# Performance work log

Hardware: AMD Instinct MI355X
Metric: run time of the kernel (lower is better)

Reference implementation:

```python
import jax, jax.numpy as jnp
import numpy as np

DIM = 1024
HEADS = 16
DIM_HEAD = 64
INNER = HEADS * DIM_HEAD
EPS = 1e-6


def elu_feature_map(t):
    # F.elu(x) + 1
    return jnp.where(t > 0, t + 1.0, jnp.exp(t))


def setup_inputs() -> dict:
    key = jax.random.key(0)
    k1, k2, k3, k4 = jax.random.split(key, 4)
    B, N = 4, 8192
    x = jax.random.normal(k1, (B, N, DIM), dtype=jnp.float32)
    s_in = 1.0 / np.sqrt(DIM)
    s_out = 1.0 / np.sqrt(INNER)
    Wqkv = jax.random.uniform(k2, (DIM, 3 * INNER), dtype=jnp.float32, minval=-s_in, maxval=s_in)
    Wout = jax.random.uniform(k3, (INNER, DIM), dtype=jnp.float32, minval=-s_out, maxval=s_out)
    bout = jax.random.uniform(k4, (DIM,), dtype=jnp.float32, minval=-s_out, maxval=s_out)
    return {"x": x, "Wqkv": Wqkv, "Wout": Wout, "bout": bout}


def reference(x, Wqkv, Wout, bout):
    B, N, D = x.shape
    qkv = x @ Wqkv  # [B,N,3*INNER]
    q, k, v = jnp.split(qkv, 3, axis=-1)
    # b n (h d) -> b h n d
    resh = lambda t: t.reshape(B, N, HEADS, DIM_HEAD).transpose(0, 2, 1, 3)
    q, k, v = resh(q), resh(k), resh(v)
    q = elu_feature_map(q)
    k = elu_feature_map(k)
    kv = jnp.einsum('bhnd,bhnf->bhdf', k, v)          # [B,H,d,d]
    k_sum = k.sum(axis=-2)                             # [B,H,d]
    qkv_out = jnp.einsum('bhnd,bhdf->bhnf', q, kv)    # [B,H,N,d]
    q_k_sum = jnp.einsum('bhnd,bhd->bhn', q, k_sum)   # [B,H,N]
    out = qkv_out / (q_k_sum[..., None] + EPS)
    out = out.transpose(0, 2, 1, 3).reshape(B, N, INNER)  # b h n d -> b n (h d)
    return out @ Wout + bout
```

## Files before the change

### kernel.cpp

```cpp
#include <hip/hip_runtime.h>
#include <hip/hip_bf16.h>
#include <math.h>


typedef unsigned short ushort_t;
typedef __attribute__((ext_vector_type(8))) short s8v;
typedef __attribute__((ext_vector_type(4))) float f32x4;

#define MFMA(a,b,c) __builtin_amdgcn_mfma_f32_16x16x32_bf16((a),(b),(c),0,0,0)

typedef __attribute__((address_space(3))) unsigned int as3_u32;
typedef __attribute__((address_space(1))) const unsigned int as1_u32c;

__device__ __forceinline__ void g2l16(const void* g, void* l) {
    __builtin_amdgcn_global_load_lds((as1_u32c*)g, (as3_u32*)l, 16, 0, 0);
}

__device__ __forceinline__ float bf2f(ushort_t u) {
    union { float f; unsigned v; } x; x.v = ((unsigned)u) << 16; return x.f;
}
__device__ __forceinline__ ushort_t f2bf(float f) {
    union { float f; unsigned v; } x; x.f = f;
    unsigned r = x.v + 0x7fffu + ((x.v >> 16) & 1u);
    return (ushort_t)(r >> 16);
}
__device__ __forceinline__ float elu1(float t) { return t > 0.0f ? t + 1.0f : expf(t); }

__global__ void k_cast(const float* __restrict__ in, ushort_t* __restrict__ out, int n8) {
    int i = blockIdx.x * blockDim.x + threadIdx.x;
    if (i >= n8) return;
    const float4* p = (const float4*)in;
    float4 a = p[(size_t)i * 2], b = p[(size_t)i * 2 + 1];
    uint4 o;
    o.x = (unsigned)f2bf(a.x) | ((unsigned)f2bf(a.y) << 16);
    o.y = (unsigned)f2bf(a.z) | ((unsigned)f2bf(a.w) << 16);
    o.z = (unsigned)f2bf(b.x) | ((unsigned)f2bf(b.y) << 16);
    o.w = (unsigned)f2bf(b.z) | ((unsigned)f2bf(b.w) << 16);
    *(uint4*)(out + (size_t)i * 8) = o;
}

__global__ __launch_bounds__(256) void k_transpose(const float* __restrict__ W,
                                                   ushort_t* __restrict__ WT, int K, int N) {
    __shared__ float s[32][33];
    const int t = threadIdx.x;
    const int k0 = blockIdx.x * 32, n0 = blockIdx.y * 32;
    const int kr = t >> 3, n4 = (t & 7) * 4;
    float4 v = *(const float4*)(W + (size_t)(k0 + kr) * N + n0 + n4);
    s[kr][n4 + 0] = v.x; s[kr][n4 + 1] = v.y; s[kr][n4 + 2] = v.z; s[kr][n4 + 3] = v.w;
    __syncthreads();
    const int nr = kr, k4 = n4;
    unsigned lo = (unsigned)f2bf(s[k4 + 0][nr]) | ((unsigned)f2bf(s[k4 + 1][nr]) << 16);
    unsigned hi = (unsigned)f2bf(s[k4 + 2][nr]) | ((unsigned)f2bf(s[k4 + 3][nr]) << 16);
    *(uint2*)(WT + (size_t)(n0 + nr) * K + k0 + k4) = make_uint2(lo, hi);
}

template<int MODE>
__global__ __launch_bounds__(512, 2) void k_gemm(
    const ushort_t* __restrict__ A, const ushort_t* __restrict__ B,
    ushort_t* __restrict__ obf, const float* __restrict__ bout, float* __restrict__ of)
{
    constexpr int ASZ  = 256 * 64;
    constexpr int BUFS = 2 * ASZ;
    __shared__ ushort_t lds[2 * BUFS];

    const int t = threadIdx.x, l = t & 63, w = t >> 6;
    const int wr = w >> 2, wc = w & 3;
    const size_t m0 = (size_t)blockIdx.x * 256;
    const size_t n0 = (size_t)blockIdx.y * 256;

    f32x4 acc[8][4];
    const f32x4 z = {0.f, 0.f, 0.f, 0.f};
#pragma unroll
    for (int i = 0; i < 8; i++)
#pragma unroll
        for (int j = 0; j < 4; j++) acc[i][j] = z;

    const int lr  = l >> 3;
    const int lco = ((l & 7) ^ lr) << 3;
    const ushort_t* gA = A + (m0 + (size_t)(32 * w) + lr) * 1024 + lco;
    const ushort_t* gB = B + (n0 + (size_t)(32 * w) + lr) * 1024 + lco;
    const int la15 = l & 15;
    const int exo  = (((l >> 4) ^ (l & 7)) << 3);

#pragma unroll
    for (int i = 0; i < 4; i++)
        g2l16(gA + (size_t)(8 * i) * 1024, &lds[(w * 4 + i) * 512]);
#pragma unroll
    for (int i = 0; i < 4; i++)
        g2l16(gB + (size_t)(8 * i) * 1024, &lds[ASZ + (w * 4 + i) * 512]);
    asm volatile("s_waitcnt vmcnt(0)" ::: "memory");
    __builtin_amdgcn_sched_barrier(0);
    __builtin_amdgcn_s_barrier();
    __builtin_amdgcn_sched_barrier(0);

    for (int T = 0; T < 16; ++T) {
        const int base  = (T & 1) * BUFS;
        const int nbase = BUFS - base;

        if (T < 15) {
            const size_t k1 = (size_t)(T + 1) * 64;
#pragma unroll
            for (int i = 0; i < 4; i++)
                g2l16(gA + (size_t)(8 * i) * 1024 + k1, &lds[nbase + (w * 4 + i) * 512]);
#pragma unroll
            for (int i = 0; i < 4; i++)
                g2l16(gB + (size_t)(8 * i) * 1024 + k1, &lds[nbase + ASZ + (w * 4 + i) * 512]);
        }

        s8v af[8], bf[4];
#pragma unroll
        for (int nf = 0; nf < 4; nf++)
            bf[nf] = *(const s8v*)&lds[base + ASZ + (wc * 64 + nf * 16 + la15) * 64 + exo];
#pragma unroll
        for (int mf = 0; mf < 8; mf++)
            af[mf] = *(const s8v*)&lds[base + (wr * 128 + mf * 16 + la15) * 64 + exo];
        __builtin_amdgcn_s_setprio(1);
#pragma unroll
        for (int mf = 0; mf < 8; mf++)
#pragma unroll
            for (int nf = 0; nf < 4; nf++)
                acc[mf][nf] = MFMA(af[mf], bf[nf], acc[mf][nf]);
        __builtin_amdgcn_s_setprio(0);
#pragma unroll
        for (int nf = 0; nf < 4; nf++)
            bf[nf] = *(const s8v*)&lds[base + ASZ + (wc * 64 + nf * 16 + la15) * 64 + (32 ^ exo)];
#pragma unroll
        for (int mf = 0; mf < 8; mf++)
            af[mf] = *(const s8v*)&lds[base + (wr * 128 + mf * 16 + la15) * 64 + (32 ^ exo)];
        __builtin_amdgcn_s_setprio(1);
#pragma unroll
        for (int mf = 0; mf < 8; mf++)
#pragma unroll
            for (int nf = 0; nf < 4; nf++)
                acc[mf][nf] = MFMA(af[mf], bf[nf], acc[mf][nf]);
        __builtin_amdgcn_s_setprio(0);

        if (T < 15) {
            __builtin_amdgcn_sched_barrier(0);
            asm volatile("s_waitcnt vmcnt(0)" ::: "memory");
            __builtin_amdgcn_sched_barrier(0);
            __builtin_amdgcn_s_barrier();
            __builtin_amdgcn_sched_barrier(0);
        }
    }

    const int r4 = (l >> 4) * 4;
    if (MODE == 0) {
#pragma unroll
        for (int mf = 0; mf < 8; mf++)
#pragma unroll
            for (int nf = 0; nf < 4; nf++) {
                const size_t colb = n0 + wc * 64 + nf * 16;
                const bool feat = colb < 2048;
#pragma unroll
                for (int r = 0; r < 4; r++) {
                    const size_t row = m0 + wr * 128 + mf * 16 + r4 + r;
                    float v = acc[mf][nf][r];
                    obf[row * 3072 + colb + la15] = f2bf(feat ? elu1(v) : v);
                }
            }
    } else {
#pragma unroll
        for (int mf = 0; mf < 8; mf++)
#pragma unroll
            for (int nf = 0; nf < 4; nf++) {
                const size_t col = n0 + wc * 64 + nf * 16 + la15;
                const float bo = bout[col];
#pragma unroll
                for (int r = 0; r < 4; r++) {
                    const size_t row = m0 + wr * 128 + mf * 16 + r4 + r;
                    of[row * 1024 + col] = acc[mf][nf][r] + bo;
                }
            }
    }
}

#define KST 136
__global__ __launch_bounds__(256) void k_kv(
    const ushort_t* __restrict__ qkv, float* __restrict__ kv, float* __restrict__ ksum)
{
    __shared__ ushort_t kT[64 * KST];
    __shared__ ushort_t vT[64 * KST];
    __shared__ float ksl[64];
    const int t = threadIdx.x, l = t & 63, w = t >> 6;
    const int wr = w >> 1, wc = w & 1;
    const int h = blockIdx.x;
    const int b = blockIdx.z;
    const ushort_t* qkvb = qkv + (size_t)b * 8192 * 3072;
    float* kvh = kv + ((size_t)b * 16 + h) * 4096;
    float* ksh = ksum + (size_t)b * 1024 + h * 64;
    const int n00 = blockIdx.y * 512;
    const f32x4 z = {0.f, 0.f, 0.f, 0.f};
    f32x4 acc[2][2] = {{z, z}, {z, z}};
    float ksloc[4] = {0.f, 0.f, 0.f, 0.f};
    const int sd0 = (t & 15) * 4;
    if (t < 64) ksl[t] = 0.f;

    for (int c = 0; c < 4; c++) {
        __syncthreads();
        const int n0 = n00 + c * 128;
#pragma unroll
        for (int i = 0; i < 8; i++) {
            int n = i * 16 + (t >> 4);
            const ushort_t* kp = qkvb + (size_t)(n0 + n) * 3072 + 1024 + h * 64 + sd0;
            ushort4 kw = *(const ushort4*)kp;
            ushort4 vw = *(const ushort4*)(kp + 1024);
            ksloc[0] += bf2f(kw.x); ksloc[1] += bf2f(kw.y);
            ksloc[2] += bf2f(kw.z); ksloc[3] += bf2f(kw.w);
            kT[(sd0 + 0) * KST + n] = kw.x; kT[(sd0 + 1) * KST + n] = kw.y;
            kT[(sd0 + 2) * KST + n] = kw.z; kT[(sd0 + 3) * KST + n] = kw.w;
            vT[(sd0 + 0) * KST + n] = vw.x; vT[(sd0 + 1) * KST + n] = vw.y;
            vT[(sd0 + 2) * KST + n] = vw.z; vT[(sd0 + 3) * KST + n] = vw.w;
        }
        __syncthreads();
#pragma unroll
        for (int kb = 0; kb < 128; kb += 32) {
            s8v af[2], bfr[2];
#pragma unroll
            for (int ma = 0; ma < 2; ma++) {
                int d = wr * 32 + ma * 16 + (l & 15);
                af[ma] = *(const s8v*)&kT[d * KST + kb + (l >> 4) * 8];
            }
#pragma unroll
            for (int fb = 0; fb < 2; fb++) {
                int f = wc * 32 + fb * 16 + (l & 15);
                bfr[fb] = *(const s8v*)&vT[f * KST + kb + (l >> 4) * 8];
            }
#pragma unroll
            for (int ma = 0; ma < 2; ma++)
#pragma unroll
                for (int fb = 0; fb < 2; fb++)
                    acc[ma][fb] = MFMA(af[ma], bfr[fb], acc[ma][fb]);
        }
    }
    atomicAdd(&ksl[sd0 + 0], ksloc[0]); atomicAdd(&ksl[sd0 + 1], ksloc[1]);
    atomicAdd(&ksl[sd0 + 2], ksloc[2]); atomicAdd(&ksl[sd0 + 3], ksloc[3]);
    __syncthreads();
    if (t < 64) atomicAdd(&ksh[t], ksl[t]);
#pragma unroll
    for (int ma = 0; ma < 2; ma++)
#pragma unroll
        for (int fb = 0; fb < 2; fb++)
#pragma unroll
            for (int r = 0; r < 4; r++) {
                int d = wr * 32 + ma * 16 + (l >> 4) * 4 + r;
                int f = wc * 32 + fb * 16 + (l & 15);
                atomicAdd(&kvh[f * 64 + d], acc[ma][fb][r]);
            }
}

#define AST 72
__global__ __launch_bounds__(256) void k_apply(
    const ushort_t* __restrict__ qkv, const float* __restrict__ kv,
    const float* __restrict__ ksum, ushort_t* __restrict__ attn)
{
    __shared__ ushort_t kvb[64 * AST];
    const int t = threadIdx.x, l = t & 63, w = t >> 6;
    const int la15 = l & 15;
    const int row0 = blockIdx.x * 32;
    const int b = row0 >> 13;
    const f32x4 z = {0.f, 0.f, 0.f, 0.f};

    for (int hh = 0; hh < 8; hh++) {
        const int h = blockIdx.y * 8 + hh;
        const float* kvh = kv + ((size_t)b * 16 + h) * 4096;
        const float* ksh = ksum + (size_t)b * 1024 + h * 64;
        __syncthreads();
        {
            const int f = t >> 2, d0 = (t & 3) * 16;
            const float* src = kvh + f * 64 + d0;
            s8v v0, v1;
#pragma unroll
            for (int j = 0; j < 8; j++) {
                v0[j] = (short)f2bf(src[j]);
                v1[j] = (short)f2bf(src[j + 8]);
            }
            *(s8v*)&kvb[f * AST + d0]     = v0;
            *(s8v*)&kvb[f * AST + d0 + 8] = v1;
        }
        __syncthreads();
        float ksv[16];
        {
            const float* kp = ksh + (l >> 4) * 8;
            *(float4*)&ksv[0]  = *(const float4*)(kp);
            *(float4*)&ksv[4]  = *(const float4*)(kp + 4);
            *(float4*)&ksv[8]  = *(const float4*)(kp + 32);
            *(float4*)&ksv[12] = *(const float4*)(kp + 36);
        }
        f32x4 acc[2] = {z, z};
        float pd[2] = {0.f, 0.f};
#pragma unroll
        for (int ks = 0; ks < 2; ks++) {
            const int f = w * 16 + la15;
            s8v bfr = *(const s8v*)&kvb[f * AST + ks * 32 + (l >> 4) * 8];
#pragma unroll
            for (int ma = 0; ma < 2; ma++) {
                int row = row0 + ma * 16 + la15;
                s8v afr = *(const s8v*)(qkv + (size_t)row * 3072 + h * 64 + ks * 32 + (l >> 4) * 8);
#pragma unroll
                for (int j = 0; j < 8; j++)
                    pd[ma] += bf2f((ushort_t)afr[j]) * ksv[ks * 8 + j];
                acc[ma] = MFMA(afr, bfr, acc[ma]);
            }
        }
#pragma unroll
        for (int ma = 0; ma < 2; ma++) {
            pd[ma] += __shfl_xor(pd[ma], 16, 64);
            pd[ma] += __shfl_xor(pd[ma], 32, 64);
        }
#pragma unroll
        for (int ma = 0; ma < 2; ma++)
#pragma unroll
            for (int r = 0; r < 4; r++) {
                int lrow = (l >> 4) * 4 + r;
                float dot = __shfl(pd[ma], lrow, 64);
                float dv = 1.f / (dot + 1e-6f);
                int row = row0 + ma * 16 + lrow;
                int f = w * 16 + la15;
                attn[(size_t)row * 1024 + h * 64 + f] = f2bf(acc[ma][r] * dv);
            }
    }
}

extern "C" void kernel_launch(void* const* d_in, const int* in_sizes, int n_in,
                              void* d_out, int out_size, void* d_ws, size_t ws_size,
                              hipStream_t stream) {
    const float* x    = (const float*)d_in[0];
    const float* Wqkv = (const float*)d_in[1];
    const float* Wout = (const float*)d_in[2];
    const float* bout = (const float*)d_in[3];
    float* out = (float*)d_out;
    char* ws = (char*)d_ws;

    ushort_t* WqkvT = (ushort_t*)(ws + 0);
    ushort_t* WoutT = (ushort_t*)(ws + 6291456);
    float*    kv    = (float*)(ws + 8388608);
    float*    ksum  = (float*)(ws + 12582912);
    ushort_t* xb    = (ushort_t*)(ws + 12599296);
    ushort_t* qkv   = (ushort_t*)(ws + 79708160);
    ushort_t* attn  = (ushort_t*)(ws + 281034752);

    k_transpose<<<dim3(32, 96), 256, 0, stream>>>(Wqkv, WqkvT, 1024, 3072);
    k_transpose<<<dim3(32, 32), 256, 0, stream>>>(Wout, WoutT, 1024, 1024);
    hipMemsetAsync(kv, 0, 4194304 + 16384, stream);
    k_cast<<<16384, 256, 0, stream>>>(x, xb, 4194304);

    k_gemm<0><<<dim3(128, 12), 512, 0, stream>>>(xb, WqkvT, qkv, nullptr, nullptr);
    k_kv<<<dim3(16, 16, 4), 256, 0, stream>>>(qkv, kv, ksum);
    k_apply<<<dim3(1024, 2), 256, 0, stream>>>(qkv, kv, ksum, attn);
    k_gemm<1><<<dim3(128, 4), 512, 0, stream>>>(attn, WoutT, nullptr, bout, out);
}
```

Before: 518.3 us.

## Remap GEMM blocks across XCDs, vectorize kv LDS stores, stage apply output

The GEMM kernels switch to a 1D grid and remap block IDs so that consecutive tiles on each of the 8 XCDs share A rows, aiming to improve L2 reuse. k_kv now loads four rows per thread and writes the transposed K/V tiles to LDS as ushort4 vectors instead of scalar stores. k_apply stages its 32x512 bf16 output in a new LDS buffer and writes it to global memory with coalesced 16-byte stores instead of scattered 2-byte stores. The extra 33 KB of LDS in k_apply may reduce occupancy.

```diff
diff --git a/kernel.cpp b/kernel.cpp
--- a/kernel.cpp
+++ b/kernel.cpp
@@ -61,12 +61,16 @@
 {
     constexpr int ASZ  = 256 * 64;
     constexpr int BUFS = 2 * ASZ;
+    constexpr int NBN  = (MODE == 0) ? 12 : 4;
+    constexpr int CH   = (128 * NBN) / 8;
     __shared__ ushort_t lds[2 * BUFS];
 
     const int t = threadIdx.x, l = t & 63, w = t >> 6;
     const int wr = w >> 2, wc = w & 3;
-    const size_t m0 = (size_t)blockIdx.x * 256;
-    const size_t n0 = (size_t)blockIdx.y * 256;
+    const int orig = blockIdx.x;
+    const int wg   = (orig & 7) * CH + (orig >> 3);
+    const size_t m0 = (size_t)(wg / NBN) * 256;
+    const size_t n0 = (size_t)(wg % NBN) * 256;
 
     f32x4 acc[8][4];
     const f32x4 z = {0.f, 0.f, 0.f, 0.f};
@@ -194,23 +198,35 @@
     f32x4 acc[2][2] = {{z, z}, {z, z}};
     float ksloc[4] = {0.f, 0.f, 0.f, 0.f};
     const int sd0 = (t & 15) * 4;
+    const int tg  = t >> 4;
     if (t < 64) ksl[t] = 0.f;
 
     for (int c = 0; c < 4; c++) {
         __syncthreads();
         const int n0 = n00 + c * 128;
 #pragma unroll
-        for (int i = 0; i < 8; i++) {
-            int n = i * 16 + (t >> 4);
-            const ushort_t* kp = qkvb + (size_t)(n0 + n) * 3072 + 1024 + h * 64 + sd0;
-            ushort4 kw = *(const ushort4*)kp;
-            ushort4 vw = *(const ushort4*)(kp + 1024);
-            ksloc[0] += bf2f(kw.x); ksloc[1] += bf2f(kw.y);
-            ksloc[2] += bf2f(kw.z); ksloc[3] += bf2f(kw.w);
-            kT[(sd0 + 0) * KST + n] = kw.x; kT[(sd0 + 1) * KST + n] = kw.y;
-            kT[(sd0 + 2) * KST + n] = kw.z; kT[(sd0 + 3) * KST + n] = kw.w;
-            vT[(sd0 + 0) * KST + n] = vw.x; vT[(sd0 + 1) * KST + n] = vw.y;
-            vT[(sd0 + 2) * KST + n] = vw.z; vT[(sd0 + 3) * KST + n] = vw.w;
+        for (int jj = 0; jj < 2; jj++) {
+            const int nb = tg * 8 + jj * 4;
+            ushort4 kw[4], vw[4];
+#pragma unroll
+            for (int j = 0; j < 4; j++) {
+                const ushort_t* kp = qkvb + (size_t)(n0 + nb + j) * 3072 + 1024 + h * 64 + sd0;
+                kw[j] = *(const ushort4*)kp;
+                vw[j] = *(const ushort4*)(kp + 1024);
+            }
+#pragma unroll
+            for (int j = 0; j < 4; j++) {
+                ksloc[0] += bf2f(kw[j].x); ksloc[1] += bf2f(kw[j].y);
+                ksloc[2] += bf2f(kw[j].z); ksloc[3] += bf2f(kw[j].w);
+            }
+            *(ushort4*)&kT[(sd0 + 0) * KST + nb] = make_ushort4(kw[0].x, kw[1].x, kw[2].x, kw[3].x);
+            *(ushort4*)&kT[(sd0 + 1) * KST + nb] = make_ushort4(kw[0].y, kw[1].y, kw[2].y, kw[3].y);
+            *(ushort4*)&kT[(sd0 + 2) * KST + nb] = make_ushort4(kw[0].z, kw[1].z, kw[2].z, kw[3].z);
+            *(ushort4*)&kT[(sd0 + 3) * KST + nb] = make_ushort4(kw[0].w, kw[1].w, kw[2].w, kw[3].w);
+            *(ushort4*)&vT[(sd0 + 0) * KST + nb] = make_ushort4(vw[0].x, vw[1].x, vw[2].x, vw[3].x);
+            *(ushort4*)&vT[(sd0 + 1) * KST + nb] = make_ushort4(vw[0].y, vw[1].y, vw[2].y, vw[3].y);
+            *(ushort4*)&vT[(sd0 + 2) * KST + nb] = make_ushort4(vw[0].z, vw[1].z, vw[2].z, vw[3].z);
+            *(ushort4*)&vT[(sd0 + 3) * KST + nb] = make_ushort4(vw[0].w, vw[1].w, vw[2].w, vw[3].w);
         }
         __syncthreads();
 #pragma unroll
@@ -250,11 +266,13 @@
 }
 
 #define AST 72
+#define OST 520
 __global__ __launch_bounds__(256) void k_apply(
     const ushort_t* __restrict__ qkv, const float* __restrict__ kv,
     const float* __restrict__ ksum, ushort_t* __restrict__ attn)
 {
     __shared__ ushort_t kvb[64 * AST];
+    __shared__ ushort_t obuf[32 * OST];
     const int t = threadIdx.x, l = t & 63, w = t >> 6;
     const int la15 = l & 15;
     const int row0 = blockIdx.x * 32;
@@ -315,10 +333,21 @@
                 int lrow = (l >> 4) * 4 + r;
                 float dot = __shfl(pd[ma], lrow, 64);
                 float dv = 1.f / (dot + 1e-6f);
-                int row = row0 + ma * 16 + lrow;
-                int f = w * 16 + la15;
-                attn[(size_t)row * 1024 + h * 64 + f] = f2bf(acc[ma][r] * dv);
-            }
+                int orow = ma * 16 + lrow;
+                int ocol = hh * 64 + w * 16 + la15;
+                obuf[orow * OST + ocol] = f2bf(acc[ma][r] * dv);
+            }
+    }
+    __syncthreads();
+    {
+        const int row = t >> 3;
+        const int c0  = (t & 7) * 8;
+        ushort_t* dst = attn + (size_t)(row0 + row) * 1024 + blockIdx.y * 512;
+#pragma unroll
+        for (int i = 0; i < 8; i++) {
+            const int col = c0 + i * 64;
+            *(uint4*)(dst + col) = *(const uint4*)&obuf[row * OST + col];
+        }
     }
 }
 
@@ -345,8 +374,8 @@
     hipMemsetAsync(kv, 0, 4194304 + 16384, stream);
     k_cast<<<16384, 256, 0, stream>>>(x, xb, 4194304);
 
-    k_gemm<0><<<dim3(128, 12), 512, 0, stream>>>(xb, WqkvT, qkv, nullptr, nullptr);
+    k_gemm<0><<<1536, 512, 0, stream>>>(xb, WqkvT, qkv, nullptr, nullptr);
     k_kv<<<dim3(16, 16, 4), 256, 0, stream>>>(qkv, kv, ksum);
     k_apply<<<dim3(1024, 2), 256, 0, stream>>>(qkv, kv, ksum, attn);
-    k_gemm<1><<<dim3(128, 4), 512, 0, stream>>>(attn, WoutT, nullptr, bout, out);
-}
+    k_gemm<1><<<512, 512, 0, stream>>>(attn, WoutT, nullptr, bout, out);
+}
```

After: 505.6 us. 1.03x faster.
